# Performance work log

Hardware: AMD Instinct MI355X
Metric: run time of the kernel (lower is better)

The kernel has to match this reference:

```python
import jax, jax.numpy as jnp
import numpy as np

B, L, D, N = 4, 8192, 128, 32


def setup_inputs() -> dict:
    key = jax.random.key(0)
    ks = jax.random.split(key, 12)
    s = 0.05  # small init scale for stability of exp/cumsum
    return {
        "x": jax.random.normal(ks[0], (B, L, D), jnp.float32),
        "h_t_minus_1": jax.random.normal(ks[1], (B, L, D), jnp.float32),
        "A_log": jax.random.normal(ks[2], (D, N), jnp.float32),
        "D_param": jnp.ones((D,), jnp.float32),
        "W_x": jax.random.normal(ks[3], (D, 2 * N + D), jnp.float32) * s,
        "W_dt": jax.random.normal(ks[4], (D, D), jnp.float32) * s,
        "b_dt": jnp.zeros((D,), jnp.float32),
        "conv_w": jax.random.normal(ks[5], (3, D, D), jnp.float32) * s,  # (width, in, out)
        "conv_b": jnp.zeros((D,), jnp.float32),
        "W_f": jax.random.normal(ks[6], (D, D), jnp.float32) * s,
        "b_f": jnp.zeros((D,), jnp.float32),
    }


def reference(x, h_t_minus_1, A_log, D_param, W_x, W_dt, b_dt, conv_w, conv_b, W_f, b_f):
    d, n = A_log.shape
    A = -jnp.exp(A_log)  # (d, n)
    x_dbl = x @ W_x  # (b, l, d + 2n)
    delta, Bm, Cm = jnp.split(x_dbl, [d, d + n], axis=-1)
    delta = jax.nn.softplus(delta @ W_dt + b_dt)  # (b, l, d)

    # selective scan
    dA = jnp.einsum('bld,dn->bldn', delta, A)
    dB_u = jnp.einsum('bld,bld,bln->bldn', delta, h_t_minus_1, Bm)
    dA_cumsum = jnp.exp(jnp.cumsum(dA, axis=1) - dA)  # exclusive cumsum
    h_t = jnp.einsum('bldn,bln->bld', dB_u * dA_cumsum, Cm)
    h_t = h_t + h_t * D_param

    ssm_output = jax.nn.relu(h_t @ W_f + b_f)
    # causal Conv1D, kernel=3: left-pad by 2
    conv = jax.lax.conv_general_dilated(
        ssm_output, conv_w, window_strides=(1,), padding=[(2, 0)],
        dimension_numbers=('NWC', 'WIO', 'NWC')) + conv_b
    causal_output = jax.nn.relu(conv)
    fused_output = ssm_output * causal_output
    return (fused_output, h_t)
```

## Files before the change

kernel.cpp:

```cpp
#include <hip/hip_runtime.h>
#include <math.h>

typedef unsigned short u16;
typedef __attribute__((ext_vector_type(8))) short short8v;
typedef __attribute__((ext_vector_type(4))) float f32x4;

constexpr int B_  = 4;
constexpr int L_  = 8192;
constexpr int D_  = 128;
constexpr int N_  = 32;
constexpr int BL  = B_ * L_;
constexpr int CH  = 16;
constexpr int NC  = L_ / CH;
constexpr int SCH = 32;
constexpr int SNC = L_ / SCH;

__device__ inline unsigned bfr(float x) {
    unsigned u = __float_as_uint(x);
    return (u + 0x7fffu + ((u >> 16) & 1u)) >> 16;
}
__device__ inline unsigned pkbf(float a, float b) { return bfr(a) | (bfr(b) << 16); }
__device__ inline float b2f(u16 h) { return __uint_as_float(((unsigned)h) << 16); }

__global__ __launch_bounds__(512) void prep_weff(
    const float* __restrict__ Wx, const float* __restrict__ Wdt,
    u16* __restrict__ Wt0)
{
    __shared__ float wd[128 * 128];
    const int tid = threadIdx.x;
    #pragma unroll
    for (int j = 0; j < 8; ++j) {
        const int g = tid + j * 512;
        *reinterpret_cast<float4*>(&wd[g * 4]) =
            *reinterpret_cast<const float4*>(&Wdt[(size_t)g * 4]);
    }
    __syncthreads();
    const int k = blockIdx.x * 4 + (tid >> 7);
    const int d = tid & 127;
    float s = 0.f;
    #pragma unroll 8
    for (int j = 0; j < 128; ++j)
        s = fmaf(Wx[(size_t)k * 192 + j], wd[j * 128 + d], s);
    Wt0[d * 128 + k] = (u16)bfr(s);
}

__global__ __launch_bounds__(256) void prep_rest(
    const float* __restrict__ Wx, const float* __restrict__ Wf,
    const float* __restrict__ Wconv, const float* __restrict__ A_log,
    u16* __restrict__ Wt0, u16* __restrict__ Wt2, u16* __restrict__ Wtc,
    float* __restrict__ negAT, float* __restrict__ amax)
{
    const int which = blockIdx.y;
    const int t = blockIdx.x * 256 + threadIdx.x;
    constexpr float L2E = 1.4426950408889634f;
    if (which == 0) {
        if (t >= 64 * 128) return;
        const int n = t >> 7, k = t & 127;
        Wt0[(128 + n) * 128 + k] = (u16)bfr(Wx[(size_t)k * 192 + 128 + n]);
    } else if (which == 1) {
        if (t >= 128 * 128) return;
        const int n = t >> 7, k = t & 127;
        Wt2[n * 128 + k] = (u16)bfr(Wf[(size_t)k * 128 + n]);
    } else if (which <= 4) {
        if (t >= 128 * 128) return;
        const int w = which - 2;
        const int n = t >> 7, k = t & 127;
        Wtc[((size_t)w * 128 + n) * 128 + k] = (u16)bfr(Wconv[((size_t)w * 128 + k) * 128 + n]);
    } else if (which == 5) {
        if (t >= 128 * 32) return;
        const int d = t >> 5, n = t & 31;
        negAT[n * 128 + d] = -expf(A_log[d * 32 + n]) * L2E;
    } else {
        if (t >= 128) return;
        float m = -1e30f;
        for (int n = 0; n < 32; ++n)
            m = fmaxf(m, -expf(A_log[t * 32 + n]) * L2E);
        amax[t] = m;
    }
}

__global__ __launch_bounds__(512) void gemm1(
    const float* __restrict__ x, const u16* __restrict__ Wt0,
    const float* __restrict__ b_dt,
    float* __restrict__ delta, float* __restrict__ bc,
    float* __restrict__ part)
{
    __shared__ __align__(16) u16 Blds[192 * 128];

    const int tid = threadIdx.x;
    const int R0 = blockIdx.x * 128;

    #pragma unroll
    for (int j = 0; j < 6; ++j) {
        const int g = tid + j * 512;
        const int n = g >> 4, k8 = (g & 15) * 8;
        const uint4 p = *reinterpret_cast<const uint4*>(&Wt0[(size_t)n * 128 + k8]);
        *reinterpret_cast<uint4*>(&Blds[n * 128 + (k8 ^ ((n & 7) << 3))]) = p;
    }

    const int w = tid >> 6, lane = tid & 63;
    const int lr = lane & 15, kg = lane >> 4;
    const int arow = R0 + w * 16 + lr;

    float4 av[4][2];
    #pragma unroll
    for (int ks = 0; ks < 4; ++ks) {
        const float* src = &x[(size_t)arow * 128 + ks * 32 + kg * 8];
        av[ks][0] = *reinterpret_cast<const float4*>(src);
        av[ks][1] = *reinterpret_cast<const float4*>(src + 4);
    }
    __syncthreads();

    f32x4 acc[12] = {};
    #pragma unroll
    for (int ks = 0; ks < 4; ++ks) {
        uint4 ap;
        ap.x = pkbf(av[ks][0].x, av[ks][0].y);
        ap.y = pkbf(av[ks][0].z, av[ks][0].w);
        ap.z = pkbf(av[ks][1].x, av[ks][1].y);
        ap.w = pkbf(av[ks][1].z, av[ks][1].w);
        const short8v af = *reinterpret_cast<const short8v*>(&ap);
        const int kb = ks * 32 + kg * 8;
        #pragma unroll
        for (int nf = 0; nf < 12; ++nf) {
            const int n = nf * 16 + lr;
            const short8v bf = *reinterpret_cast<const short8v*>(
                &Blds[n * 128 + (kb ^ ((n & 7) << 3))]);
            acc[nf] = __builtin_amdgcn_mfma_f32_16x16x32_bf16(af, bf, acc[nf], 0, 0, 0);
        }
    }

    const int orow = R0 + w * 16;
    const int bb = orow >> 13;
    const int chk = (orow & (L_ - 1)) >> 4;
    #pragma unroll
    for (int nf = 0; nf < 8; ++nf) {
        const int col = nf * 16 + lr;
        const float bbv = b_dt[col];
        float v[4];
        #pragma unroll
        for (int q = 0; q < 4; ++q) {
            const float t = acc[nf][q] + bbv;
            v[q] = fmaxf(t, 0.f) + log1pf(expf(-fabsf(t)));
        }
        const float g4 = v[0] + v[1] + v[2] + v[3];
        const float g0 = __shfl(g4, lr, 64);
        const float g1 = __shfl(g4, lr + 16, 64);
        const float g2 = __shfl(g4, lr + 32, 64);
        const float g3 = __shfl(g4, lr + 48, 64);
        const size_t rb = (size_t)(orow + kg * 4) * 128 + col;
        delta[rb + 0 * 128] = v[0];
        delta[rb + 1 * 128] = v[1];
        delta[rb + 2 * 128] = v[2];
        delta[rb + 3 * 128] = v[3];
        if (kg == 0)
            part[((size_t)bb * 128 + col) * NC + chk] = g0 + g1 + g2 + g3;
    }
    #pragma unroll
    for (int h2 = 0; h2 < 2; ++h2)
        #pragma unroll
        for (int q = 0; q < 4; ++q)
            bc[(size_t)(orow + kg * 4 + q) * 32 + h2 * 16 + lr] =
                acc[8 + h2][q] * acc[10 + h2][q];
}

__global__ __launch_bounds__(512) void scan_prefix(float* __restrict__ part)
{
    const int b = blockIdx.x, d = blockIdx.y;
    const int c = threadIdx.x, w = c >> 6, lane = c & 63;
    const size_t base = ((size_t)b * 128 + d) * NC;
    const float v = part[base + c];
    float s = v;
    #pragma unroll
    for (int off = 1; off < 64; off <<= 1) {
        const float t = __shfl_up(s, off, 64);
        if (lane >= off) s += t;
    }
    __shared__ float wsum[8];
    if (lane == 63) wsum[w] = s;
    __syncthreads();
    float add = 0.f;
    #pragma unroll
    for (int i = 0; i < 8; ++i)
        if (i < w) add += wsum[i];
    part[base + c] = s + add - v;
}

__global__ __launch_bounds__(512) void scan_main(
    const float* __restrict__ delta, const float* __restrict__ hprev,
    const float* __restrict__ bc, const float* __restrict__ negAT,
    const float* __restrict__ amax, const float* __restrict__ Dp,
    const float* __restrict__ part,
    const u16* __restrict__ Wt2, const float* __restrict__ b_f,
    float* __restrict__ h_out, u16* __restrict__ ssm)
{
    __shared__ float delta_s[SCH * 128];
    __shared__ float at_s[32 * 128];
    __shared__ float bc_s[SCH * 32];
    __shared__ __align__(16) u16 h_s[SCH * 128];

    const int cb = blockIdx.x, b = blockIdx.y;
    const int tid = threadIdx.x;
    const size_t rowbase = (size_t)b * L_ + (size_t)cb * SCH;

    #pragma unroll
    for (int j = 0; j < 2; ++j) {
        const int g = tid + j * 512;
        reinterpret_cast<float4*>(delta_s)[g] =
            reinterpret_cast<const float4*>(&delta[rowbase * 128])[g];
    }
    #pragma unroll
    for (int j = 0; j < 2; ++j) {
        const int g = tid + j * 512;
        reinterpret_cast<float4*>(at_s)[g] =
            reinterpret_cast<const float4*>(negAT)[g];
    }
    if (tid < 256)
        reinterpret_cast<float4*>(bc_s)[tid] =
            reinterpret_cast<const float4*>(&bc[rowbase * 32])[tid];

    const int d = tid & 127, r0 = tid >> 7;
    const float dp1 = 1.f + Dp[d];
    const float am = amax[d];
    const size_t pb = ((size_t)b * 128 + d) * NC + (size_t)cb * 2;
    const float part0 = part[pb];
    const float part1 = part[pb + 1];
    __syncthreads();

    float sv[8];
    {
        float s = part0;
        #pragma unroll
        for (int i = 0; i < 16; ++i) {
            if ((i & 3) == r0) sv[i >> 2] = s;
            s += delta_s[i * 128 + d];
        }
        s = part1;
        #pragma unroll
        for (int i = 16; i < 32; ++i) {
            if ((i & 3) == r0) sv[i >> 2] = s;
            s += delta_s[i * 128 + d];
        }
    }

    #pragma unroll 1
    for (int r = 0; r < 8; ++r) {
        const int row = r * 4 + r0;
        const size_t rb = (rowbase + row) * 128 + d;
        const float S = sv[r];
        float h = 0.f;
        if (__any(S * am >= -80.f)) {
            const float dv = delta_s[row * 128 + d];
            const float hv = hprev[rb];
            float p0 = 0.f, p1 = 0.f, p2 = 0.f, p3 = 0.f;
            #pragma unroll
            for (int n4 = 0; n4 < 8; ++n4) {
                const float4 b4 = *reinterpret_cast<const float4*>(&bc_s[row * 32 + n4 * 4]);
                p0 = fmaf(b4.x, exp2f(S * at_s[(n4 * 4 + 0) * 128 + d]), p0);
                p1 = fmaf(b4.y, exp2f(S * at_s[(n4 * 4 + 1) * 128 + d]), p1);
                p2 = fmaf(b4.z, exp2f(S * at_s[(n4 * 4 + 2) * 128 + d]), p2);
                p3 = fmaf(b4.w, exp2f(S * at_s[(n4 * 4 + 3) * 128 + d]), p3);
            }
            h = dv * hv * ((p0 + p1) + (p2 + p3)) * dp1;
        }
        h_out[rb] = h;
        h_s[row * 128 + (d ^ ((row & 7) << 3))] = (u16)bfr(h);
    }
    __syncthreads();

    const int wid = tid >> 6, lane = tid & 63;
    const int lr = lane & 15, kg = lane >> 4;
    const int col = wid * 16 + lr;
    f32x4 acc[2] = {};
    #pragma unroll
    for (int ks = 0; ks < 4; ++ks) {
        const int k8 = ks * 32 + kg * 8;
        const short8v bfg = *reinterpret_cast<const short8v*>(&Wt2[(size_t)col * 128 + k8]);
        #pragma unroll
        for (int m = 0; m < 2; ++m) {
            const int row = m * 16 + lr;
            const short8v afg = *reinterpret_cast<const short8v*>(
                &h_s[row * 128 + (k8 ^ ((row & 7) << 3))]);
            acc[m] = __builtin_amdgcn_mfma_f32_16x16x32_bf16(afg, bfg, acc[m], 0, 0, 0);
        }
    }
    const float bb = b_f[col];
    #pragma unroll
    for (int m = 0; m < 2; ++m)
        #pragma unroll
        for (int q = 0; q < 4; ++q) {
            const int row = m * 16 + kg * 4 + q;
            const float v = fmaxf(acc[m][q] + bb, 0.f);
            ssm[(rowbase + row) * 128 + col] = (u16)bfr(v);
        }
}

__global__ __launch_bounds__(512) void conv_fuse(
    const u16* __restrict__ ssm, const u16* __restrict__ Wtc,
    const float* __restrict__ cbias, float* __restrict__ fused)
{
    __shared__ __align__(16) u16 Alds[66 * 128];

    const int tid = threadIdx.x;
    const int bb = blockIdx.y;
    const int r0 = blockIdx.x * 64;
    const u16* sb = ssm + (size_t)bb * L_ * 128;

    #pragma unroll
    for (int j = 0; j < 3; ++j) {
        const int g = tid + j * 512;
        if (g < 66 * 16) {
            const int i = g >> 4, k8 = (g & 15) * 8;
            const int gr = r0 - 2 + i;
            uint4 p = make_uint4(0, 0, 0, 0);
            if (gr >= 0)
                p = *reinterpret_cast<const uint4*>(&sb[(size_t)gr * 128 + k8]);
            *reinterpret_cast<uint4*>(&Alds[i * 128 + (k8 ^ ((i & 7) << 3))]) = p;
        }
    }
    __syncthreads();

    const int wid = tid >> 6, lane = tid & 63;
    const int wm = wid >> 2, wn = wid & 3;
    const int lr = lane & 15, kg = lane >> 4;

    f32x4 acc[2][2] = {};
    #pragma unroll
    for (int ks = 0; ks < 4; ++ks) {
        const int k8 = ks * 32 + kg * 8;
        short8v af[2][3];
        #pragma unroll
        for (int m = 0; m < 2; ++m)
            #pragma unroll
            for (int w = 0; w < 3; ++w) {
                const int ri = wm * 32 + m * 16 + lr + w;
                af[m][w] = *reinterpret_cast<const short8v*>(
                    &Alds[ri * 128 + (k8 ^ ((ri & 7) << 3))]);
            }
        #pragma unroll
        for (int nf = 0; nf < 2; ++nf) {
            const int col = wn * 32 + nf * 16 + lr;
            #pragma unroll
            for (int w = 0; w < 3; ++w) {
                const short8v bfg = *reinterpret_cast<const short8v*>(
                    &Wtc[((size_t)w * 128 + col) * 128 + k8]);
                acc[0][nf] = __builtin_amdgcn_mfma_f32_16x16x32_bf16(af[0][w], bfg, acc[0][nf], 0, 0, 0);
                acc[1][nf] = __builtin_amdgcn_mfma_f32_16x16x32_bf16(af[1][w], bfg, acc[1][nf], 0, 0, 0);
            }
        }
    }

    #pragma unroll
    for (int nf = 0; nf < 2; ++nf) {
        const int col = wn * 32 + nf * 16 + lr;
        const float bb2 = cbias[col];
        #pragma unroll
        for (int m = 0; m < 2; ++m)
            #pragma unroll
            for (int q = 0; q < 4; ++q) {
                const int row = wm * 32 + m * 16 + kg * 4 + q;
                const int ri = row + 2;
                const u16 sh = Alds[ri * 128 + ((((col >> 3) ^ (ri & 7)) << 3)) + (col & 7)];
                const float cv = fmaxf(acc[m][nf][q] + bb2, 0.f);
                fused[((size_t)bb * L_ + r0 + row) * 128 + col] = b2f(sh) * cv;
            }
    }
}

extern "C" void kernel_launch(void* const* d_in, const int* in_sizes, int n_in,
                              void* d_out, int out_size, void* d_ws, size_t ws_size,
                              hipStream_t stream)
{
    const float* x      = (const float*)d_in[0];
    const float* hprev  = (const float*)d_in[1];
    const float* A_log  = (const float*)d_in[2];
    const float* Dp     = (const float*)d_in[3];
    const float* W_x    = (const float*)d_in[4];
    const float* W_dt   = (const float*)d_in[5];
    const float* b_dt   = (const float*)d_in[6];
    const float* conv_w = (const float*)d_in[7];
    const float* conv_b = (const float*)d_in[8];
    const float* W_f    = (const float*)d_in[9];
    const float* b_f    = (const float*)d_in[10];

    float* out   = (float*)d_out;
    float* h_out = out + (size_t)BL * D_;

    char* ws = (char*)d_ws;
    float* delta = (float*)ws;                  ws += (size_t)BL * 128 * 4;
    float* bcb   = (float*)ws;                  ws += (size_t)BL * 32 * 4;
    float* part  = (float*)ws;                  ws += (size_t)B_ * 128 * NC * 4;
    float* negAT = (float*)ws;                  ws += (size_t)N_ * 128 * 4;
    float* amaxb = (float*)ws;                  ws += (size_t)128 * 4;
    u16*   Wt0   = (u16*)ws;                    ws += (size_t)192 * 128 * 2;
    u16*   Wt2   = (u16*)ws;                    ws += (size_t)128 * 128 * 2;
    u16*   Wtc   = (u16*)ws;                    ws += (size_t)3 * 128 * 128 * 2;
    u16*   ssm   = (u16*)ws;

    prep_weff<<<dim3(32), dim3(512), 0, stream>>>(W_x, W_dt, Wt0);
    prep_rest<<<dim3(64, 7), dim3(256), 0, stream>>>(
        W_x, W_f, conv_w, A_log, Wt0, Wt2, Wtc, negAT, amaxb);
    gemm1<<<dim3(BL / 128), dim3(512), 0, stream>>>(
        x, Wt0, b_dt, delta, bcb, part);
    scan_prefix<<<dim3(B_, D_), dim3(512), 0, stream>>>(part);
    scan_main<<<dim3(SNC, B_), dim3(512), 0, stream>>>(
        delta, hprev, bcb, negAT, amaxb, Dp, part, Wt2, b_f, h_out, ssm);
    conv_fuse<<<dim3(L_ / 64, B_), dim3(512), 0, stream>>>(
        ssm, Wtc, conv_b, out);
}
```

Measured before the change: 168.9 us.

## Merge prep kernels, fuse chunk prefix into scan, move W_f GEMM into conv kernel

```diff
diff --git a/kernel.cpp b/kernel.cpp
--- a/kernel.cpp
+++ b/kernel.cpp
@@ -22,51 +22,50 @@
 __device__ inline unsigned pkbf(float a, float b) { return bfr(a) | (bfr(b) << 16); }
 __device__ inline float b2f(u16 h) { return __uint_as_float(((unsigned)h) << 16); }
 
-__global__ __launch_bounds__(512) void prep_weff(
+__global__ __launch_bounds__(512) void prep(
     const float* __restrict__ Wx, const float* __restrict__ Wdt,
-    u16* __restrict__ Wt0)
-{
-    __shared__ float wd[128 * 128];
-    const int tid = threadIdx.x;
-    #pragma unroll
-    for (int j = 0; j < 8; ++j) {
-        const int g = tid + j * 512;
-        *reinterpret_cast<float4*>(&wd[g * 4]) =
-            *reinterpret_cast<const float4*>(&Wdt[(size_t)g * 4]);
-    }
-    __syncthreads();
-    const int k = blockIdx.x * 4 + (tid >> 7);
-    const int d = tid & 127;
-    float s = 0.f;
-    #pragma unroll 8
-    for (int j = 0; j < 128; ++j)
-        s = fmaf(Wx[(size_t)k * 192 + j], wd[j * 128 + d], s);
-    Wt0[d * 128 + k] = (u16)bfr(s);
-}
-
-__global__ __launch_bounds__(256) void prep_rest(
-    const float* __restrict__ Wx, const float* __restrict__ Wf,
-    const float* __restrict__ Wconv, const float* __restrict__ A_log,
+    const float* __restrict__ Wf, const float* __restrict__ Wconv,
+    const float* __restrict__ A_log,
     u16* __restrict__ Wt0, u16* __restrict__ Wt2, u16* __restrict__ Wtc,
     float* __restrict__ negAT, float* __restrict__ amax)
 {
-    const int which = blockIdx.y;
-    const int t = blockIdx.x * 256 + threadIdx.x;
+    const int y = blockIdx.y;
+    const int tid = threadIdx.x;
     constexpr float L2E = 1.4426950408889634f;
-    if (which == 0) {
+    if (y == 0) {
+        if (blockIdx.x >= 32) return;
+        __shared__ float wd[128 * 128];
+        #pragma unroll
+        for (int j = 0; j < 8; ++j) {
+            const int g = tid + j * 512;
+            *reinterpret_cast<float4*>(&wd[g * 4]) =
+                *reinterpret_cast<const float4*>(&Wdt[(size_t)g * 4]);
+        }
+        __syncthreads();
+        const int k = blockIdx.x * 4 + (tid >> 7);
+        const int d = tid & 127;
+        float s = 0.f;
+        #pragma unroll 8
+        for (int j = 0; j < 128; ++j)
+            s = fmaf(Wx[(size_t)k * 192 + j], wd[j * 128 + d], s);
+        Wt0[d * 128 + k] = (u16)bfr(s);
+        return;
+    }
+    const int t = blockIdx.x * 512 + tid;
+    if (y == 1) {
         if (t >= 64 * 128) return;
         const int n = t >> 7, k = t & 127;
         Wt0[(128 + n) * 128 + k] = (u16)bfr(Wx[(size_t)k * 192 + 128 + n]);
-    } else if (which == 1) {
+    } else if (y == 2) {
         if (t >= 128 * 128) return;
         const int n = t >> 7, k = t & 127;
         Wt2[n * 128 + k] = (u16)bfr(Wf[(size_t)k * 128 + n]);
-    } else if (which <= 4) {
+    } else if (y <= 5) {
         if (t >= 128 * 128) return;
-        const int w = which - 2;
+        const int w = y - 3;
         const int n = t >> 7, k = t & 127;
         Wtc[((size_t)w * 128 + n) * 128 + k] = (u16)bfr(Wconv[((size_t)w * 128 + k) * 128 + n]);
-    } else if (which == 5) {
+    } else if (y == 6) {
         if (t >= 128 * 32) return;
         const int d = t >> 5, n = t & 31;
         negAT[n * 128 + d] = -expf(A_log[d * 32 + n]) * L2E;
@@ -79,7 +78,7 @@
     }
 }
 
-__global__ __launch_bounds__(512) void gemm1(
+__global__ __launch_bounds__(256) void gemm1(
     const float* __restrict__ x, const u16* __restrict__ Wt0,
     const float* __restrict__ b_dt,
     float* __restrict__ delta, float* __restrict__ bc,
@@ -88,11 +87,11 @@
     __shared__ __align__(16) u16 Blds[192 * 128];
 
     const int tid = threadIdx.x;
-    const int R0 = blockIdx.x * 128;
-
-    #pragma unroll
-    for (int j = 0; j < 6; ++j) {
-        const int g = tid + j * 512;
+    const int r0 = blockIdx.x * 64;
+
+    #pragma unroll
+    for (int j = 0; j < 12; ++j) {
+        const int g = tid + j * 256;
         const int n = g >> 4, k8 = (g & 15) * 8;
         const uint4 p = *reinterpret_cast<const uint4*>(&Wt0[(size_t)n * 128 + k8]);
         *reinterpret_cast<uint4*>(&Blds[n * 128 + (k8 ^ ((n & 7) << 3))]) = p;
@@ -100,7 +99,7 @@
 
     const int w = tid >> 6, lane = tid & 63;
     const int lr = lane & 15, kg = lane >> 4;
-    const int arow = R0 + w * 16 + lr;
+    const int arow = r0 + w * 16 + lr;
 
     float4 av[4][2];
     #pragma unroll
@@ -130,7 +129,7 @@
         }
     }
 
-    const int orow = R0 + w * 16;
+    const int orow = r0 + w * 16;
     const int bb = orow >> 13;
     const int chk = (orow & (L_ - 1)) >> 4;
     #pragma unroll
@@ -164,40 +163,17 @@
                 acc[8 + h2][q] * acc[10 + h2][q];
 }
 
-__global__ __launch_bounds__(512) void scan_prefix(float* __restrict__ part)
-{
-    const int b = blockIdx.x, d = blockIdx.y;
-    const int c = threadIdx.x, w = c >> 6, lane = c & 63;
-    const size_t base = ((size_t)b * 128 + d) * NC;
-    const float v = part[base + c];
-    float s = v;
-    #pragma unroll
-    for (int off = 1; off < 64; off <<= 1) {
-        const float t = __shfl_up(s, off, 64);
-        if (lane >= off) s += t;
-    }
-    __shared__ float wsum[8];
-    if (lane == 63) wsum[w] = s;
-    __syncthreads();
-    float add = 0.f;
-    #pragma unroll
-    for (int i = 0; i < 8; ++i)
-        if (i < w) add += wsum[i];
-    part[base + c] = s + add - v;
-}
-
 __global__ __launch_bounds__(512) void scan_main(
     const float* __restrict__ delta, const float* __restrict__ hprev,
     const float* __restrict__ bc, const float* __restrict__ negAT,
     const float* __restrict__ amax, const float* __restrict__ Dp,
     const float* __restrict__ part,
-    const u16* __restrict__ Wt2, const float* __restrict__ b_f,
-    float* __restrict__ h_out, u16* __restrict__ ssm)
+    float* __restrict__ h_out, u16* __restrict__ hb)
 {
     __shared__ float delta_s[SCH * 128];
     __shared__ float at_s[32 * 128];
     __shared__ float bc_s[SCH * 32];
-    __shared__ __align__(16) u16 h_s[SCH * 128];
+    __shared__ float P_lds[128 * 2];
 
     const int cb = blockIdx.x, b = blockIdx.y;
     const int tid = threadIdx.x;
@@ -219,13 +195,34 @@
         reinterpret_cast<float4*>(bc_s)[tid] =
             reinterpret_cast<const float4*>(&bc[rowbase * 32])[tid];
 
+    {
+        const int dq = tid >> 2, j = tid & 3;
+        const size_t pb = ((size_t)b * 128 + dq) * NC;
+        const int Cend = cb * 2;
+        float e0 = 0.f, e1 = 0.f;
+        int c = j;
+        for (; c + 4 < Cend; c += 8) {
+            e0 += part[pb + c];
+            e1 += part[pb + c + 4];
+        }
+        for (; c < Cend; c += 4) e0 += part[pb + c];
+        float e = e0 + e1;
+        e += __shfl_xor(e, 1, 64);
+        e += __shfl_xor(e, 2, 64);
+        if (j == 0) {
+            const float extra = part[pb + Cend];
+            P_lds[dq * 2]     = e;
+            P_lds[dq * 2 + 1] = e + extra;
+        }
+    }
+
     const int d = tid & 127, r0 = tid >> 7;
     const float dp1 = 1.f + Dp[d];
     const float am = amax[d];
-    const size_t pb = ((size_t)b * 128 + d) * NC + (size_t)cb * 2;
-    const float part0 = part[pb];
-    const float part1 = part[pb + 1];
     __syncthreads();
+
+    const float part0 = P_lds[d * 2];
+    const float part1 = P_lds[d * 2 + 1];
 
     float sv[8];
     {
@@ -264,66 +261,68 @@
             h = dv * hv * ((p0 + p1) + (p2 + p3)) * dp1;
         }
         h_out[rb] = h;
-        h_s[row * 128 + (d ^ ((row & 7) << 3))] = (u16)bfr(h);
-    }
-    __syncthreads();
-
-    const int wid = tid >> 6, lane = tid & 63;
-    const int lr = lane & 15, kg = lane >> 4;
-    const int col = wid * 16 + lr;
-    f32x4 acc[2] = {};
-    #pragma unroll
-    for (int ks = 0; ks < 4; ++ks) {
-        const int k8 = ks * 32 + kg * 8;
-        const short8v bfg = *reinterpret_cast<const short8v*>(&Wt2[(size_t)col * 128 + k8]);
-        #pragma unroll
-        for (int m = 0; m < 2; ++m) {
-            const int row = m * 16 + lr;
-            const short8v afg = *reinterpret_cast<const short8v*>(
-                &h_s[row * 128 + (k8 ^ ((row & 7) << 3))]);
-            acc[m] = __builtin_amdgcn_mfma_f32_16x16x32_bf16(afg, bfg, acc[m], 0, 0, 0);
-        }
-    }
-    const float bb = b_f[col];
-    #pragma unroll
-    for (int m = 0; m < 2; ++m)
-        #pragma unroll
-        for (int q = 0; q < 4; ++q) {
-            const int row = m * 16 + kg * 4 + q;
-            const float v = fmaxf(acc[m][q] + bb, 0.f);
-            ssm[(rowbase + row) * 128 + col] = (u16)bfr(v);
-        }
-}
-
-__global__ __launch_bounds__(512) void conv_fuse(
-    const u16* __restrict__ ssm, const u16* __restrict__ Wtc,
+        hb[rb] = (u16)bfr(h);
+    }
+}
+
+__global__ __launch_bounds__(512) void conv_fuse2(
+    const u16* __restrict__ hb, const u16* __restrict__ Wt2,
+    const float* __restrict__ b_f, const u16* __restrict__ Wtc,
     const float* __restrict__ cbias, float* __restrict__ fused)
 {
-    __shared__ __align__(16) u16 Alds[66 * 128];
+    __shared__ __align__(16) u16 hb_s[80 * 128];
+    __shared__ __align__(16) u16 ssm_s[80 * 128];
 
     const int tid = threadIdx.x;
     const int bb = blockIdx.y;
     const int r0 = blockIdx.x * 64;
-    const u16* sb = ssm + (size_t)bb * L_ * 128;
+    const u16* hbB = hb + (size_t)bb * L_ * 128;
 
     #pragma unroll
     for (int j = 0; j < 3; ++j) {
         const int g = tid + j * 512;
-        if (g < 66 * 16) {
-            const int i = g >> 4, k8 = (g & 15) * 8;
-            const int gr = r0 - 2 + i;
+        if (g < 80 * 16) {
+            const int s = g >> 4, k8 = (g & 15) * 8;
+            const int gr = r0 - 2 + s;
             uint4 p = make_uint4(0, 0, 0, 0);
-            if (gr >= 0)
-                p = *reinterpret_cast<const uint4*>(&sb[(size_t)gr * 128 + k8]);
-            *reinterpret_cast<uint4*>(&Alds[i * 128 + (k8 ^ ((i & 7) << 3))]) = p;
+            if (gr >= 0 && gr < L_)
+                p = *reinterpret_cast<const uint4*>(&hbB[(size_t)gr * 128 + k8]);
+            *reinterpret_cast<uint4*>(&hb_s[s * 128 + (k8 ^ ((s & 7) << 3))]) = p;
         }
     }
     __syncthreads();
 
-    const int wid = tid >> 6, lane = tid & 63;
-    const int wm = wid >> 2, wn = wid & 3;
+    const int w = tid >> 6, lane = tid & 63;
     const int lr = lane & 15, kg = lane >> 4;
 
+    #pragma unroll
+    for (int ui = 0; ui < 5; ++ui) {
+        const int u = w * 5 + ui;
+        const int sm = u >> 3, nf = u & 7;
+        const int col = nf * 16 + lr;
+        f32x4 a = {};
+        #pragma unroll
+        for (int ks = 0; ks < 4; ++ks) {
+            const int kb = ks * 32 + kg * 8;
+            const int sr = sm * 16 + lr;
+            const short8v af = *reinterpret_cast<const short8v*>(
+                &hb_s[sr * 128 + (kb ^ ((sr & 7) << 3))]);
+            const short8v bf = *reinterpret_cast<const short8v*>(
+                &Wt2[(size_t)col * 128 + kb]);
+            a = __builtin_amdgcn_mfma_f32_16x16x32_bf16(af, bf, a, 0, 0, 0);
+        }
+        const float bbv = b_f[col];
+        #pragma unroll
+        for (int q = 0; q < 4; ++q) {
+            const int s2 = sm * 16 + kg * 4 + q;
+            float vv = fmaxf(a[q] + bbv, 0.f);
+            if (r0 - 2 + s2 < 0) vv = 0.f;
+            ssm_s[s2 * 128 + (col ^ ((s2 & 7) << 3))] = (u16)bfr(vv);
+        }
+    }
+    __syncthreads();
+
+    const int wm = w >> 2, wn = w & 3;
     f32x4 acc[2][2] = {};
     #pragma unroll
     for (int ks = 0; ks < 4; ++ks) {
@@ -332,37 +331,36 @@
         #pragma unroll
         for (int m = 0; m < 2; ++m)
             #pragma unroll
-            for (int w = 0; w < 3; ++w) {
-                const int ri = wm * 32 + m * 16 + lr + w;
-                af[m][w] = *reinterpret_cast<const short8v*>(
-                    &Alds[ri * 128 + (k8 ^ ((ri & 7) << 3))]);
+            for (int t = 0; t < 3; ++t) {
+                const int ri = wm * 32 + m * 16 + lr + t;
+                af[m][t] = *reinterpret_cast<const short8v*>(
+                    &ssm_s[ri * 128 + (k8 ^ ((ri & 7) << 3))]);
             }
         #pragma unroll
         for (int nf = 0; nf < 2; ++nf) {
             const int col = wn * 32 + nf * 16 + lr;
             #pragma unroll
-            for (int w = 0; w < 3; ++w) {
+            for (int t = 0; t < 3; ++t) {
                 const short8v bfg = *reinterpret_cast<const short8v*>(
-                    &Wtc[((size_t)w * 128 + col) * 128 + k8]);
-                acc[0][nf] = __builtin_amdgcn_mfma_f32_16x16x32_bf16(af[0][w], bfg, acc[0][nf], 0, 0, 0);
-                acc[1][nf] = __builtin_amdgcn_mfma_f32_16x16x32_bf16(af[1][w], bfg, acc[1][nf], 0, 0, 0);
+                    &Wtc[((size_t)t * 128 + col) * 128 + k8]);
+                acc[0][nf] = __builtin_amdgcn_mfma_f32_16x16x32_bf16(af[0][t], bfg, acc[0][nf], 0, 0, 0);
+                acc[1][nf] = __builtin_amdgcn_mfma_f32_16x16x32_bf16(af[1][t], bfg, acc[1][nf], 0, 0, 0);
             }
         }
     }
-
     #pragma unroll
     for (int nf = 0; nf < 2; ++nf) {
         const int col = wn * 32 + nf * 16 + lr;
-        const float bb2 = cbias[col];
+        const float cb2 = cbias[col];
         #pragma unroll
         for (int m = 0; m < 2; ++m)
             #pragma unroll
             for (int q = 0; q < 4; ++q) {
-                const int row = wm * 32 + m * 16 + kg * 4 + q;
-                const int ri = row + 2;
-                const u16 sh = Alds[ri * 128 + ((((col >> 3) ^ (ri & 7)) << 3)) + (col & 7)];
-                const float cv = fmaxf(acc[m][nf][q] + bb2, 0.f);
-                fused[((size_t)bb * L_ + r0 + row) * 128 + col] = b2f(sh) * cv;
+                const int ro = wm * 32 + m * 16 + kg * 4 + q;
+                const int ri = ro + 2;
+                const u16 sh = ssm_s[ri * 128 + (col ^ ((ri & 7) << 3))];
+                const float cv = fmaxf(acc[m][nf][q] + cb2, 0.f);
+                fused[((size_t)bb * L_ + r0 + ro) * 128 + col] = b2f(sh) * cv;
             }
     }
 }
@@ -395,16 +393,14 @@
     u16*   Wt0   = (u16*)ws;                    ws += (size_t)192 * 128 * 2;
     u16*   Wt2   = (u16*)ws;                    ws += (size_t)128 * 128 * 2;
     u16*   Wtc   = (u16*)ws;                    ws += (size_t)3 * 128 * 128 * 2;
-    u16*   ssm   = (u16*)ws;
-
-    prep_weff<<<dim3(32), dim3(512), 0, stream>>>(W_x, W_dt, Wt0);
-    prep_rest<<<dim3(64, 7), dim3(256), 0, stream>>>(
-        W_x, W_f, conv_w, A_log, Wt0, Wt2, Wtc, negAT, amaxb);
-    gemm1<<<dim3(BL / 128), dim3(512), 0, stream>>>(
+    u16*   hb    = (u16*)ws;
+
+    prep<<<dim3(64, 8), dim3(512), 0, stream>>>(
+        W_x, W_dt, W_f, conv_w, A_log, Wt0, Wt2, Wtc, negAT, amaxb);
+    gemm1<<<dim3(BL / 64), dim3(256), 0, stream>>>(
         x, Wt0, b_dt, delta, bcb, part);
-    scan_prefix<<<dim3(B_, D_), dim3(512), 0, stream>>>(part);
     scan_main<<<dim3(SNC, B_), dim3(512), 0, stream>>>(
-        delta, hprev, bcb, negAT, amaxb, Dp, part, Wt2, b_f, h_out, ssm);
-    conv_fuse<<<dim3(L_ / 64, B_), dim3(512), 0, stream>>>(
-        ssm, Wtc, conv_b, out);
-}
+        delta, hprev, bcb, negAT, amaxb, Dp, part, h_out, hb);
+    conv_fuse2<<<dim3(L_ / 64, B_), dim3(512), 0, stream>>>(
+        hb, Wt2, b_f, Wtc, conv_b, out);
+}
```

New measurement: 183.3 us. 8.5% more time.
